# Kernel tuning notes

Hardware: AMD Instinct MI355X
Metric: run time of the kernel (lower is better)

Reference implementation:

```python
import jax, jax.numpy as jnp
import numpy as np

D_MODEL, D_K, D_V = 512, 64, 64


def setup_inputs() -> dict:
    key = jax.random.key(0)
    ks = jax.random.split(key, 9)
    b, n = 8, 4096
    scale = 1.0 / np.sqrt(D_MODEL)
    return {
        "q": jax.random.normal(ks[0], (b, n, D_MODEL), jnp.float32),
        "k": jax.random.normal(ks[1], (b, n, D_MODEL), jnp.float32),
        "v": jax.random.normal(ks[2], (b, n, D_MODEL), jnp.float32),
        "Wq": jax.random.normal(ks[3], (D_MODEL, D_K), jnp.float32) * scale,
        "bq": jnp.zeros((D_K,), jnp.float32),
        "Wk": jax.random.normal(ks[4], (D_MODEL, D_K), jnp.float32) * scale,
        "bk": jnp.zeros((D_K,), jnp.float32),
        "Wv": jax.random.normal(ks[5], (D_MODEL, D_V), jnp.float32) * scale,
        "bv": jnp.zeros((D_V,), jnp.float32),
        "mask": 0,
    }


def reference(q, k, v, Wq, bq, Wk, bk, Wv, bv, mask):
    # linear projections (torch Linear: x @ W^T + b; here W stored as [in,out])
    qp = jnp.einsum("bnd,de->bne", q, Wq) + bq  # (b,n,d_k)
    kp = jnp.einsum("bnd,de->bne", k, Wk) + bk  # (b,n,d_k)
    vp = jnp.einsum("bnd,de->bne", v, Wv) + bv  # (b,n,d_v)
    temper = D_K ** 0.5
    attn = jnp.einsum("bqe,bke->bqk", qp, kp) / temper  # (b,n,n)
    # original: attn[attn == mask] = -inf (equality mask on scores)
    attn = jnp.where(attn == jnp.float32(mask), -jnp.inf, attn)
    # NOTE: original's `attn.masked_fill(look_ahead_mask==0, -inf)` is NOT
    # in-place and its result is discarded, so look_ahead_mask has no effect.
    attn = jax.nn.softmax(attn, axis=-1)
    return jnp.einsum("bqk,bkv->bqv", attn, vp)  # (b,n,d_v)
```

## Files before the change

kernel.cpp:

```cpp
#include <hip/hip_runtime.h>

typedef _Float16 f16;
typedef _Float16 f16x2 __attribute__((ext_vector_type(2)));
typedef _Float16 f16x4 __attribute__((ext_vector_type(4)));
typedef _Float16 f16x8 __attribute__((ext_vector_type(8)));
typedef __fp16   h16x2 __attribute__((ext_vector_type(2)));
typedef float    f32x4 __attribute__((ext_vector_type(4)));
typedef float    f32x16 __attribute__((ext_vector_type(16)));

static constexpr float L2E = 1.44269504088896340736f;
static constexpr float QSC = 0.18033688011112042f;

static __device__ __forceinline__ f32x4 mfma16(f16x8 a, f16x8 b, f32x4 c) {
    return __builtin_amdgcn_mfma_f32_16x16x32_f16(a, b, c, 0, 0, 0);
}
static __device__ __forceinline__ f32x16 mfma32(f16x8 a, f16x8 b, f32x16 c) {
    return __builtin_amdgcn_mfma_f32_32x32x16_f16(a, b, c, 0, 0, 0);
}
static __device__ __forceinline__ f16x2 cvt_pk(float a, float b) {
    h16x2 t = __builtin_amdgcn_cvt_pkrtz(a, b);
    return __builtin_bit_cast(f16x2, t);
}
static __device__ __forceinline__ void gload16(const void* g, void* l) {
    __builtin_amdgcn_global_load_lds(
        (const __attribute__((address_space(1))) unsigned int*)g,
        (__attribute__((address_space(3))) unsigned int*)l, 16, 0, 0);
}

__global__ void ah_wt_prep(const float* __restrict__ Wq,
                           const float* __restrict__ Wk,
                           const float* __restrict__ Wv,
                           f16* __restrict__ WT) {
    const float* W = (blockIdx.x == 0) ? Wq : (blockIdx.x == 1) ? Wk : Wv;
    f16* o = WT + (size_t)blockIdx.x * (64 * 512);
    for (int i = threadIdx.x; i < 64 * 512; i += blockDim.x) {
        int col = i >> 9, e = i & 511;
        o[i] = (f16)W[e * 64 + col];
    }
}

__global__ __launch_bounds__(256, 2) void ah_proj(
    const float* __restrict__ Xq, const float* __restrict__ Xk, const float* __restrict__ Xv,
    const float* __restrict__ bq, const float* __restrict__ bk, const float* __restrict__ bv,
    const f16* __restrict__ WT,
    f16* __restrict__ qp, f16* __restrict__ kp, f16* __restrict__ vpT) {

    const int tens = blockIdx.y;
    const float* X    = (tens == 0) ? Xq : (tens == 1) ? Xk : Xv;
    const float* bias = (tens == 0) ? bq : (tens == 1) ? bk : bv;
    const f16* wt = WT + (size_t)tens * (64 * 512);
    const float osc = (tens == 0) ? QSC : 1.0f;

    const int lane = threadIdx.x & 63;
    const int wave = threadIdx.x >> 6;
    const int l15 = lane & 15, g = lane >> 4;
    const int row0 = blockIdx.x * 64;

    __shared__ __align__(16) f16 wlds[64 * 520];

    {
        int t = threadIdx.x;
        int row = t >> 2, q = t & 3;
        const f16* src = wt + (size_t)row * 512 + q * 128;
        f16* dst = &wlds[row * 520 + q * 128];
#pragma unroll
        for (int i = 0; i < 16; ++i)
            *(f16x8*)(dst + i * 8) = *(const f16x8*)(src + i * 8);
    }
    __syncthreads();

    f32x4 acc[4];
#pragma unroll
    for (int b = 0; b < 4; ++b) acc[b] = (f32x4){0.f, 0.f, 0.f, 0.f};

    const float* xrow = X + (size_t)(row0 + wave * 16 + l15) * 512;

#pragma unroll 4
    for (int ec = 0; ec < 16; ++ec) {
        const float* px = xrow + ec * 32 + g * 8;
        float4 v0 = *(const float4*)px;
        float4 v1 = *(const float4*)(px + 4);
        f16x2 p0 = cvt_pk(v0.x, v0.y), p1 = cvt_pk(v0.z, v0.w);
        f16x2 p2 = cvt_pk(v1.x, v1.y), p3 = cvt_pk(v1.z, v1.w);
        f16x8 a;
        a[0] = p0[0]; a[1] = p0[1]; a[2] = p1[0]; a[3] = p1[1];
        a[4] = p2[0]; a[5] = p2[1]; a[6] = p3[0]; a[7] = p3[1];
#pragma unroll
        for (int cf = 0; cf < 4; ++cf) {
            f16x8 bfr = *(const f16x8*)(&wlds[(cf * 16 + l15) * 520 + (ec * 4 + g) * 8]);
            acc[cf] = mfma16(a, bfr, acc[cf]);
        }
    }

    __syncthreads();

    f16* lds = wlds;
#pragma unroll
    for (int cf = 0; cf < 4; ++cf) {
        float b = bias[cf * 16 + l15];
#pragma unroll
        for (int r = 0; r < 4; ++r) {
            int rr = wave * 16 + g * 4 + r;
            lds[rr * 68 + cf * 16 + l15] = (f16)((acc[cf][r] + b) * osc);
        }
    }
    __syncthreads();

    if (tens < 2) {
        f16* o = ((tens == 0) ? qp : kp) + (size_t)row0 * 64;
        for (int c = threadIdx.x; c < 64 * 16; c += 256) {
            int r = c >> 4, ch = c & 15;
            *(f16x4*)(o + r * 64 + ch * 4) = *(const f16x4*)(&lds[r * 68 + ch * 4]);
        }
    } else {
        int b = row0 >> 12, n0 = row0 & 4095;
        f16* o = vpT + (size_t)b * 64 * 4096 + n0;
        for (int c = threadIdx.x; c < 64 * 16; c += 256) {
            int d = c >> 4, nch = c & 15;
            f16x4 v;
#pragma unroll
            for (int j = 0; j < 4; ++j) v[j] = lds[(nch * 4 + j) * 68 + d];
            *(f16x4*)(o + (size_t)d * 4096 + nch * 4) = v;
        }
    }
}

__global__ __launch_bounds__(512, 2) void ah_attn(
    const f16* __restrict__ qp, const f16* __restrict__ kp, const f16* __restrict__ vpT,
    const int* __restrict__ maskp, float* __restrict__ out) {

    const int id = blockIdx.x;
    const int batch = id & 7, qtile = id >> 3;
    const int lane = threadIdx.x & 63, wave = threadIdx.x >> 6;
    const int l31 = lane & 31, hi2 = lane >> 5;
    const int s = wave & 3, qg = wave >> 2;
    const int q0 = qtile * 128 + qg * 64;
    const float mthr = L2E * (float)maskp[0];

    const f16* qpb = qp + (size_t)batch * 4096 * 64;
    const f16* kpb = kp + (size_t)batch * 4096 * 64;
    const f16* vpb = vpT + (size_t)batch * 64 * 4096;

    __shared__ __align__(16) char smem[65536];
    __shared__ float mlx[2][4][2][32];

    const int krow = lane >> 3;
    const int vrow = lane >> 2;
    const int eswzK = (lane & 7) ^ krow;
    const int eswzV = (lane & 3) ^ (vrow & 3);
    const int swzK = l31 & 7, swzV = l31 & 3;

#define STAGE(DB, IT) do {                                                          \
    const int _k0 = (((IT) * 4 + s) << 5);                                          \
    char* _b = smem + ((s * 2 + (DB)) * 8192) + (qg ? 4096 : 0);                    \
    if (qg == 0) {                                                                  \
        _Pragma("unroll")                                                           \
        for (int _j = 0; _j < 4; ++_j)                                              \
            gload16(kpb + (size_t)(_k0 + _j * 8 + krow) * 64 + eswzK * 8,           \
                    _b + _j * 1024);                                                \
    } else {                                                                        \
        _Pragma("unroll")                                                           \
        for (int _j = 0; _j < 4; ++_j)                                              \
            gload16(vpb + (size_t)(_j * 16 + vrow) * 4096 + _k0 + eswzV * 8,        \
                    _b + _j * 1024);                                                \
    }                                                                               \
} while (0)

    f16x8 qf_[2][4];
#pragma unroll
    for (int qt = 0; qt < 2; ++qt)
#pragma unroll
        for (int st = 0; st < 4; ++st)
            qf_[qt][st] = *(const f16x8*)(qpb + (size_t)(q0 + qt * 32 + l31) * 64 + st * 16 + hi2 * 8);

    f32x16 oacc[2][2];
#pragma unroll
    for (int dt = 0; dt < 2; ++dt)
#pragma unroll
        for (int qt = 0; qt < 2; ++qt)
#pragma unroll
            for (int r = 0; r < 16; ++r) oacc[dt][qt][r] = 0.f;
    float ps[2] = {0.f, 0.f};

    STAGE(0, 0);
    int db = 0;
    for (int it = 0; it < 32; ++it) {
        if (it < 31) {
            STAGE(db ^ 1, it + 1);
            asm volatile("s_waitcnt vmcnt(4)" ::: "memory");
        } else {
            asm volatile("s_waitcnt vmcnt(0)" ::: "memory");
        }
        __builtin_amdgcn_s_barrier();
        __builtin_amdgcn_sched_barrier(0);

        const char* kb = smem + (s * 2 + db) * 8192;
        const char* vb = kb + 4096;

        f16x8 ka[4];
#pragma unroll
        for (int st = 0; st < 4; ++st)
            ka[st] = *(const f16x8*)(kb + l31 * 128 + (((st * 2 + hi2) ^ swzK) << 4));
        f32x16 sacc[2];
#pragma unroll
        for (int qt = 0; qt < 2; ++qt)
#pragma unroll
            for (int r = 0; r < 16; ++r) sacc[qt][r] = 0.f;
#pragma unroll
        for (int st = 0; st < 4; ++st)
#pragma unroll
            for (int qt = 0; qt < 2; ++qt)
                sacc[qt] = mfma32(ka[st], qf_[qt][st], sacc[qt]);

        f16x8 av[2][2];
#pragma unroll
        for (int dt = 0; dt < 2; ++dt)
#pragma unroll
            for (int t = 0; t < 2; ++t) {
                const char* p = vb + (dt * 32 + l31) * 64 + hi2 * 8;
                *(f16x4*)(&av[dt][t])       = *(const f16x4*)(p + (((t * 2 + 0) ^ swzV) << 4));
                *((f16x4*)(&av[dt][t]) + 1) = *(const f16x4*)(p + (((t * 2 + 1) ^ swzV) << 4));
            }

        f16x8 pb_[2][2];
#pragma unroll
        for (int qt = 0; qt < 2; ++qt)
#pragma unroll
            for (int t = 0; t < 2; ++t)
#pragma unroll
                for (int w = 0; w < 4; ++w) {
                    float s0 = sacc[qt][t * 8 + 2 * w];
                    float s1 = sacc[qt][t * 8 + 2 * w + 1];
                    float e0 = __builtin_amdgcn_exp2f(s0);
                    float e1 = __builtin_amdgcn_exp2f(s1);
                    float p0 = (s0 == mthr) ? 0.f : e0;
                    float p1 = (s1 == mthr) ? 0.f : e1;
                    ps[qt] += p0 + p1;
                    ((f16x2*)(&pb_[qt][t]))[w] = cvt_pk(p0, p1);
                }

#pragma unroll
        for (int dt = 0; dt < 2; ++dt)
#pragma unroll
            for (int qt = 0; qt < 2; ++qt)
#pragma unroll
                for (int t = 0; t < 2; ++t)
                    oacc[dt][qt] = mfma32(av[dt][t], pb_[qt][t], oacc[dt][qt]);

        __builtin_amdgcn_sched_barrier(0);
        __builtin_amdgcn_s_barrier();
        __builtin_amdgcn_sched_barrier(0);
        db ^= 1;
    }
#undef STAGE

    ps[0] += __shfl_xor(ps[0], 32);
    ps[1] += __shfl_xor(ps[1], 32);
    if (lane < 32) { mlx[qg][s][0][lane] = ps[0]; mlx[qg][s][1][lane] = ps[1]; }
    __syncthreads();

    float* SC = (float*)smem;
#define SCI(B, DT, QT, R) ((((qg * 2 + (B)) * 64) + ((DT) * 2 + (QT)) * 16 + (R)) * 64 + lane)
    if (s >= 2) {
#pragma unroll
        for (int dt = 0; dt < 2; ++dt)
#pragma unroll
            for (int qt = 0; qt < 2; ++qt)
#pragma unroll
                for (int r = 0; r < 16; ++r)
                    SC[SCI(s - 2, dt, qt, r)] = oacc[dt][qt][r];
    }
    __syncthreads();
    if (s < 2) {
#pragma unroll
        for (int dt = 0; dt < 2; ++dt)
#pragma unroll
            for (int qt = 0; qt < 2; ++qt)
#pragma unroll
                for (int r = 0; r < 16; ++r)
                    oacc[dt][qt][r] += SC[SCI(s, dt, qt, r)];
        if (s == 1) {
#pragma unroll
            for (int dt = 0; dt < 2; ++dt)
#pragma unroll
                for (int qt = 0; qt < 2; ++qt)
#pragma unroll
                    for (int r = 0; r < 16; ++r)
                        SC[SCI(1, dt, qt, r)] = oacc[dt][qt][r];
        }
    }
    __syncthreads();
    if (s == 0) {
        float inv[2];
#pragma unroll
        for (int qt = 0; qt < 2; ++qt)
            inv[qt] = 1.0f / (mlx[qg][0][qt][l31] + mlx[qg][1][qt][l31] +
                              mlx[qg][2][qt][l31] + mlx[qg][3][qt][l31]);
#pragma unroll
        for (int qt = 0; qt < 2; ++qt) {
            float* o0 = out + ((size_t)batch * 4096 + q0 + qt * 32 + l31) * 64;
#pragma unroll
            for (int dt = 0; dt < 2; ++dt)
#pragma unroll
                for (int rg = 0; rg < 4; ++rg) {
                    float4 v;
                    v.x = (oacc[dt][qt][rg * 4 + 0] + SC[SCI(1, dt, qt, rg * 4 + 0)]) * inv[qt];
                    v.y = (oacc[dt][qt][rg * 4 + 1] + SC[SCI(1, dt, qt, rg * 4 + 1)]) * inv[qt];
                    v.z = (oacc[dt][qt][rg * 4 + 2] + SC[SCI(1, dt, qt, rg * 4 + 2)]) * inv[qt];
                    v.w = (oacc[dt][qt][rg * 4 + 3] + SC[SCI(1, dt, qt, rg * 4 + 3)]) * inv[qt];
                    *(float4*)(o0 + dt * 32 + rg * 8 + hi2 * 4) = v;
                }
        }
    }
#undef SCI
}

extern "C" void kernel_launch(void* const* d_in, const int* in_sizes, int n_in,
                              void* d_out, int out_size, void* d_ws, size_t ws_size,
                              hipStream_t stream) {
    const float* q  = (const float*)d_in[0];
    const float* k  = (const float*)d_in[1];
    const float* v  = (const float*)d_in[2];
    const float* Wq = (const float*)d_in[3];
    const float* bq = (const float*)d_in[4];
    const float* Wk = (const float*)d_in[5];
    const float* bk = (const float*)d_in[6];
    const float* Wv = (const float*)d_in[7];
    const float* bv = (const float*)d_in[8];
    const int* mask = (const int*)d_in[9];
    float* out = (float*)d_out;

    const size_t NTOK = (size_t)8 * 4096;
    f16* qp  = (f16*)d_ws;
    f16* kp  = qp + NTOK * 64;
    f16* vpT = kp + NTOK * 64;
    f16* WT  = vpT + NTOK * 64;

    ah_wt_prep<<<dim3(3), 256, 0, stream>>>(Wq, Wk, Wv, WT);
    ah_proj<<<dim3(512, 3), 256, 0, stream>>>(q, k, v, bq, bk, bv, WT, qp, kp, vpT);
    ah_attn<<<dim3(256), 512, 0, stream>>>(qp, kp, vpT, mask, out);
}
```

Baseline: 127.1 us.

## Stream projection X rows through per-wave LDS ring with async global_load_lds

Changes the projection kernel to stage X rows into a per-wave double-buffered LDS ring using direct global-to-LDS loads issued two stages ahead, with explicit vmcnt waits, instead of loading float4 directly into registers. The weight tile in LDS switches from padded rows to an XOR-swizzled layout to avoid bank conflicts. The intent is to hide global load latency in the memory-bound projection, at the cost of more LDS use (80KB per block), which may lower occupancy with launch_bounds(256,2).

```diff
diff --git a/kernel.cpp b/kernel.cpp
--- a/kernel.cpp
+++ b/kernel.cpp
@@ -56,30 +56,50 @@
     const int l15 = lane & 15, g = lane >> 4;
     const int row0 = blockIdx.x * 64;
 
-    __shared__ __align__(16) f16 wlds[64 * 520];
+    __shared__ __align__(16) char smem[81920];
+    f16* wlds = (f16*)smem;
+    char* ring = smem + 65536 + wave * 4096;
 
     {
-        int t = threadIdx.x;
-        int row = t >> 2, q = t & 3;
-        const f16* src = wt + (size_t)row * 512 + q * 128;
-        f16* dst = &wlds[row * 520 + q * 128];
-#pragma unroll
-        for (int i = 0; i < 16; ++i)
-            *(f16x8*)(dst + i * 8) = *(const f16x8*)(src + i * 8);
-    }
-    __syncthreads();
+        int row = threadIdx.x >> 2, q = threadIdx.x & 3;
+        const f16* src = wt + (size_t)row * 512;
+        f16* dstrow = wlds + row * 512;
+#pragma unroll
+        for (int i = 0; i < 16; ++i) {
+            int u = q * 16 + i;
+            *(f16x8*)(dstrow + ((u ^ (row & 7)) << 3)) = *(const f16x8*)(src + u * 8);
+        }
+    }
+    __syncthreads();
+
+    const int xsu = (lane & 7) ^ ((lane >> 3) & 7);
+    const float* xbase = X + (size_t)(row0 + wave * 16 + (lane >> 3)) * 512 + xsu * 4;
+
+#define XSTAGE(EC) do {                                                   \
+    char* _d = ring + (((EC) & 1) << 11);                                 \
+    gload16(xbase + (EC) * 32, _d);                                       \
+    gload16(xbase + 8 * 512 + (EC) * 32, _d + 1024);                     \
+} while (0)
 
     f32x4 acc[4];
 #pragma unroll
     for (int b = 0; b < 4; ++b) acc[b] = (f32x4){0.f, 0.f, 0.f, 0.f};
 
-    const float* xrow = X + (size_t)(row0 + wave * 16 + l15) * 512;
-
-#pragma unroll 4
+    XSTAGE(0);
+    XSTAGE(1);
+#pragma unroll
     for (int ec = 0; ec < 16; ++ec) {
-        const float* px = xrow + ec * 32 + g * 8;
-        float4 v0 = *(const float4*)px;
-        float4 v1 = *(const float4*)(px + 4);
+        if (ec < 15) asm volatile("s_waitcnt vmcnt(2)" ::: "memory");
+        else         asm volatile("s_waitcnt vmcnt(0)" ::: "memory");
+        __builtin_amdgcn_sched_barrier(0);
+
+        const char* cb = ring + ((ec & 1) << 11) + l15 * 128;
+        float4 v0 = *(const float4*)(cb + (((g * 2)     ^ (l15 & 7)) << 4));
+        float4 v1 = *(const float4*)(cb + (((g * 2 + 1) ^ (l15 & 7)) << 4));
+        asm volatile("s_waitcnt lgkmcnt(0)" ::: "memory");
+        __builtin_amdgcn_sched_barrier(0);
+        if (ec < 14) XSTAGE(ec + 2);
+
         f16x2 p0 = cvt_pk(v0.x, v0.y), p1 = cvt_pk(v0.z, v0.w);
         f16x2 p2 = cvt_pk(v1.x, v1.y), p3 = cvt_pk(v1.z, v1.w);
         f16x8 a;
@@ -87,10 +107,13 @@
         a[4] = p2[0]; a[5] = p2[1]; a[6] = p3[0]; a[7] = p3[1];
 #pragma unroll
         for (int cf = 0; cf < 4; ++cf) {
-            f16x8 bfr = *(const f16x8*)(&wlds[(cf * 16 + l15) * 520 + (ec * 4 + g) * 8]);
+            int out = cf * 16 + l15;
+            f16x8 bfr = *(const f16x8*)(wlds + (size_t)out * 512 +
+                                        (((ec * 4 + g) ^ (out & 7)) << 3));
             acc[cf] = mfma16(a, bfr, acc[cf]);
         }
     }
+#undef XSTAGE
 
     __syncthreads();
 
```

Measured after the change: 127.7 us. Within noise of the previous version (+0.4%).

## Pipeline projection X loads through per-wave LDS ring via async global_load_lds

Applied to the files above, without the earlier changes.

The projection kernel now streams X tiles into a per-wave 8-deep LDS ring buffer using direct global-to-LDS loads with swizzled addressing, issuing loads 8 chunks ahead and gating on vmcnt. W is also loaded directly into LDS with an XOR-style rotation to avoid bank conflicts. The aim is to hide global load latency in the projection stage. The cost is 128 KB of LDS, which drops occupancy to one block per CU, and the launch bound hint is relaxed to match.

```diff
diff --git a/kernel.cpp b/kernel.cpp
--- a/kernel.cpp
+++ b/kernel.cpp
@@ -39,7 +39,7 @@
     }
 }
 
-__global__ __launch_bounds__(256, 2) void ah_proj(
+__global__ __launch_bounds__(256) void ah_proj(
     const float* __restrict__ Xq, const float* __restrict__ Xk, const float* __restrict__ Xv,
     const float* __restrict__ bq, const float* __restrict__ bk, const float* __restrict__ bv,
     const f16* __restrict__ WT,
@@ -55,52 +55,74 @@
     const int wave = threadIdx.x >> 6;
     const int l15 = lane & 15, g = lane >> 4;
     const int row0 = blockIdx.x * 64;
-
-    __shared__ __align__(16) f16 wlds[64 * 520];
-
-    {
-        int t = threadIdx.x;
-        int row = t >> 2, q = t & 3;
-        const f16* src = wt + (size_t)row * 512 + q * 128;
-        f16* dst = &wlds[row * 520 + q * 128];
-#pragma unroll
-        for (int i = 0; i < 16; ++i)
-            *(f16x8*)(dst + i * 8) = *(const f16x8*)(src + i * 8);
-    }
-    __syncthreads();
+    const int wrow = wave * 16;
+
+    __shared__ __align__(16) char smem[131072];
+    char* ring = smem + 65536 + wave * 16384;
+
+#define XST(EC) do {                                                               \
+    char* _d = ring + ((EC) & 7) * 2048;                                           \
+    int _r = lane >> 3;                                                            \
+    int _u = ((lane & 7) - _r) & 7;                                                \
+    gload16(X + (size_t)(row0 + wrow + _r) * 512 + (EC) * 32 + _u * 4, _d);        \
+    gload16(X + (size_t)(row0 + wrow + 8 + _r) * 512 + (EC) * 32 + _u * 4,         \
+            _d + 1024);                                                            \
+} while (0)
+
+#pragma unroll
+    for (int i = 0; i < 16; ++i) {
+        int r = wrow + i;
+        gload16(wt + (size_t)r * 512 + (((lane - r) & 63) << 3),
+                smem + r * 1024);
+    }
+    XST(0); XST(1); XST(2); XST(3); XST(4); XST(5); XST(6); XST(7);
+    asm volatile("s_waitcnt vmcnt(16)" ::: "memory");
+    __builtin_amdgcn_s_barrier();
+    __builtin_amdgcn_sched_barrier(0);
 
     f32x4 acc[4];
 #pragma unroll
     for (int b = 0; b < 4; ++b) acc[b] = (f32x4){0.f, 0.f, 0.f, 0.f};
 
-    const float* xrow = X + (size_t)(row0 + wave * 16 + l15) * 512;
-
-#pragma unroll 4
-    for (int ec = 0; ec < 16; ++ec) {
-        const float* px = xrow + ec * 32 + g * 8;
-        float4 v0 = *(const float4*)px;
-        float4 v1 = *(const float4*)(px + 4);
-        f16x2 p0 = cvt_pk(v0.x, v0.y), p1 = cvt_pk(v0.z, v0.w);
-        f16x2 p2 = cvt_pk(v1.x, v1.y), p3 = cvt_pk(v1.z, v1.w);
-        f16x8 a;
-        a[0] = p0[0]; a[1] = p0[1]; a[2] = p1[0]; a[3] = p1[1];
-        a[4] = p2[0]; a[5] = p2[1]; a[6] = p3[0]; a[7] = p3[1];
-#pragma unroll
-        for (int cf = 0; cf < 4; ++cf) {
-            f16x8 bfr = *(const f16x8*)(&wlds[(cf * 16 + l15) * 520 + (ec * 4 + g) * 8]);
-            acc[cf] = mfma16(a, bfr, acc[cf]);
-        }
-    }
-
-    __syncthreads();
-
-    f16* lds = wlds;
+#define PITER(EC, NW) do {                                                         \
+    asm volatile("s_waitcnt vmcnt(" #NW ")" ::: "memory");                         \
+    __builtin_amdgcn_sched_barrier(0);                                             \
+    const char* cb = ring + ((EC) & 7) * 2048 + l15 * 128;                         \
+    float4 v0 = *(const float4*)(cb + (((2 * g + 0 + l15) & 7) << 4));             \
+    float4 v1 = *(const float4*)(cb + (((2 * g + 1 + l15) & 7) << 4));             \
+    asm volatile("s_waitcnt lgkmcnt(0)" ::: "memory");                             \
+    __builtin_amdgcn_sched_barrier(0);                                             \
+    if ((EC) < 8) XST((EC) + 8);                \
+    f16x2 p0 = cvt_pk(v0.x, v0.y), p1 = cvt_pk(v0.z, v0.w);                        \
+    f16x2 p2 = cvt_pk(v1.x, v1.y), p3 = cvt_pk(v1.z, v1.w);                        \
+    f16x8 a;                                                                       \
+    a[0] = p0[0]; a[1] = p0[1]; a[2] = p1[0]; a[3] = p1[1];                        \
+    a[4] = p2[0]; a[5] = p2[1]; a[6] = p3[0]; a[7] = p3[1];                        \
+    _Pragma("unroll")                                                              \
+    for (int cf = 0; cf < 4; ++cf) {                                               \
+        int wr = cf * 16 + l15;                                                    \
+        f16x8 bfr = *(const f16x8*)(smem + wr * 1024 +                             \
+                                    ((((EC) * 4 + g + wr) & 63) << 4));            \
+        acc[cf] = mfma16(a, bfr, acc[cf]);                                         \
+    }                                                                              \
+} while (0)
+
+    PITER(0, 14);  PITER(1, 14);  PITER(2, 14);  PITER(3, 14);
+    PITER(4, 14);  PITER(5, 14);  PITER(6, 14);  PITER(7, 14);
+    PITER(8, 14);  PITER(9, 12);  PITER(10, 10); PITER(11, 8);
+    PITER(12, 6);  PITER(13, 4);  PITER(14, 2);  PITER(15, 0);
+#undef PITER
+#undef XST
+
+    __syncthreads();
+
+    f16* lds = (f16*)smem;
 #pragma unroll
     for (int cf = 0; cf < 4; ++cf) {
         float b = bias[cf * 16 + l15];
 #pragma unroll
         for (int r = 0; r < 4; ++r) {
-            int rr = wave * 16 + g * 4 + r;
+            int rr = wrow + g * 4 + r;
             lds[rr * 68 + cf * 16 + l15] = (f16)((acc[cf][r] + b) * osc);
         }
     }
```

Result: slower. 132.8 us (+4.5%).

## Pipeline projection loads through LDS with async global_load_lds ring buffer

Applied to the files above, without the earlier changes.

The projection kernel no longer preloads the whole transposed weight into LDS up front. It now streams X and W chunks through a 4-stage LDS ring using async global_load_lds, with vmcnt waits and barriers between stages and an XOR swizzle on the X tile. Occupancy is raised to 3 blocks per SM. This is meant to hide global load latency in the projection GEMM, at the cost of extra barriers per k-chunk and more complex scheduling.

```diff
diff --git a/kernel.cpp b/kernel.cpp
--- a/kernel.cpp
+++ b/kernel.cpp
@@ -39,7 +39,7 @@
     }
 }
 
-__global__ __launch_bounds__(256, 2) void ah_proj(
+__global__ __launch_bounds__(256, 3) void ah_proj(
     const float* __restrict__ Xq, const float* __restrict__ Xk, const float* __restrict__ Xv,
     const float* __restrict__ bq, const float* __restrict__ bk, const float* __restrict__ bv,
     const f16* __restrict__ WT,
@@ -55,52 +55,82 @@
     const int wave = threadIdx.x >> 6;
     const int l15 = lane & 15, g = lane >> 4;
     const int row0 = blockIdx.x * 64;
-
-    __shared__ __align__(16) f16 wlds[64 * 520];
-
-    {
-        int t = threadIdx.x;
-        int row = t >> 2, q = t & 3;
-        const f16* src = wt + (size_t)row * 512 + q * 128;
-        f16* dst = &wlds[row * 520 + q * 128];
-#pragma unroll
-        for (int i = 0; i < 16; ++i)
-            *(f16x8*)(dst + i * 8) = *(const f16x8*)(src + i * 8);
-    }
-    __syncthreads();
+    const int wrow = wave * 16;
+
+    __shared__ __align__(16) char smem[49152];
+
+    const int xr8 = lane >> 3;
+    const int xsu = (lane & 7) ^ xr8;
+
+#define PSTAGE(KC) do {                                                              \
+    char* _xb = smem + ((KC) & 3) * 12288;                                           \
+    char* _wb = _xb + 8192;                                                          \
+    gload16(X + (size_t)(row0 + wrow + xr8) * 512 + (KC) * 32 + xsu * 4,             \
+            _xb + wave * 2048);                                                      \
+    gload16(X + (size_t)(row0 + wrow + 8 + xr8) * 512 + (KC) * 32 + xsu * 4,         \
+            _xb + wave * 2048 + 1024);                                               \
+    gload16(wt + (size_t)(wrow + (lane >> 2)) * 512 + (KC) * 32 + (lane & 3) * 8,    \
+            _wb + wave * 1024);                                                      \
+} while (0)
 
     f32x4 acc[4];
 #pragma unroll
     for (int b = 0; b < 4; ++b) acc[b] = (f32x4){0.f, 0.f, 0.f, 0.f};
 
-    const float* xrow = X + (size_t)(row0 + wave * 16 + l15) * 512;
-
-#pragma unroll 4
-    for (int ec = 0; ec < 16; ++ec) {
-        const float* px = xrow + ec * 32 + g * 8;
-        float4 v0 = *(const float4*)px;
-        float4 v1 = *(const float4*)(px + 4);
-        f16x2 p0 = cvt_pk(v0.x, v0.y), p1 = cvt_pk(v0.z, v0.w);
-        f16x2 p2 = cvt_pk(v1.x, v1.y), p3 = cvt_pk(v1.z, v1.w);
-        f16x8 a;
-        a[0] = p0[0]; a[1] = p0[1]; a[2] = p1[0]; a[3] = p1[1];
-        a[4] = p2[0]; a[5] = p2[1]; a[6] = p3[0]; a[7] = p3[1];
-#pragma unroll
-        for (int cf = 0; cf < 4; ++cf) {
-            f16x8 bfr = *(const f16x8*)(&wlds[(cf * 16 + l15) * 520 + (ec * 4 + g) * 8]);
-            acc[cf] = mfma16(a, bfr, acc[cf]);
-        }
-    }
-
-    __syncthreads();
-
-    f16* lds = wlds;
+#define PCOMP(KC) do {                                                               \
+    const char* _xb = smem + ((KC) & 3) * 12288;                                     \
+    const char* _wb = _xb + 8192;                                                    \
+    const char* _cb = _xb + (wrow + l15) * 128;                                      \
+    float4 v0 = *(const float4*)(_cb + (((2 * g + 0) ^ (l15 & 7)) << 4));            \
+    float4 v1 = *(const float4*)(_cb + (((2 * g + 1) ^ (l15 & 7)) << 4));            \
+    f16x2 p0 = cvt_pk(v0.x, v0.y), p1 = cvt_pk(v0.z, v0.w);                          \
+    f16x2 p2 = cvt_pk(v1.x, v1.y), p3 = cvt_pk(v1.z, v1.w);                          \
+    f16x8 a;                                                                         \
+    a[0] = p0[0]; a[1] = p0[1]; a[2] = p1[0]; a[3] = p1[1];                          \
+    a[4] = p2[0]; a[5] = p2[1]; a[6] = p3[0]; a[7] = p3[1];                          \
+    _Pragma("unroll")                                                                \
+    for (int cf = 0; cf < 4; ++cf) {                                                 \
+        f16x8 bfr = *(const f16x8*)(_wb + (cf * 16 + l15) * 64 + g * 16);            \
+        acc[cf] = mfma16(a, bfr, acc[cf]);                                           \
+    }                                                                                \
+} while (0)
+
+    PSTAGE(0); PSTAGE(1); PSTAGE(2);
+    for (int kc = 0; kc < 13; ++kc) {
+        PSTAGE(kc + 3);
+        asm volatile("s_waitcnt vmcnt(9)" ::: "memory");
+        __builtin_amdgcn_sched_barrier(0);
+        __builtin_amdgcn_s_barrier();
+        __builtin_amdgcn_sched_barrier(0);
+        PCOMP(kc);
+        __builtin_amdgcn_sched_barrier(0);
+        __builtin_amdgcn_s_barrier();
+    }
+    asm volatile("s_waitcnt vmcnt(6)" ::: "memory");
+    __builtin_amdgcn_sched_barrier(0);
+    __builtin_amdgcn_s_barrier();
+    PCOMP(13);
+    __builtin_amdgcn_s_barrier();
+    asm volatile("s_waitcnt vmcnt(3)" ::: "memory");
+    __builtin_amdgcn_sched_barrier(0);
+    __builtin_amdgcn_s_barrier();
+    PCOMP(14);
+    __builtin_amdgcn_s_barrier();
+    asm volatile("s_waitcnt vmcnt(0)" ::: "memory");
+    __builtin_amdgcn_sched_barrier(0);
+    __builtin_amdgcn_s_barrier();
+    PCOMP(15);
+    __syncthreads();
+#undef PSTAGE
+#undef PCOMP
+
+    f16* lds = (f16*)smem;
 #pragma unroll
     for (int cf = 0; cf < 4; ++cf) {
         float b = bias[cf * 16 + l15];
 #pragma unroll
         for (int r = 0; r < 4; ++r) {
-            int rr = wave * 16 + g * 4 + r;
+            int rr = wrow + g * 4 + r;
             lds[rr * 68 + cf * 16 + l15] = (f16)((acc[cf][r] + b) * osc);
         }
     }
```

Result: faster. 115.8 us (-8.9%).
